# Performance work log

Measured on AMD Instinct MI355X. Metric: run time of the kernel, lower is better.

## Reference

```python
import jax, jax.numpy as jnp
import numpy as np

B, T, H, W, C = 4, 128, 100, 464, 128
VOCAB, EMB, HID = 30000, 300, 600


def lstm(x, Wx, Wh, b):
    # Keras LSTM, gate order i, f, c, o; returns all hidden states [B,T,HID]
    bsz = x.shape[0]
    xg = jnp.einsum('bte,eg->btg', x, Wx) + b  # precompute input contribution

    def step(carry, xg_t):
        h, c = carry
        g = xg_t + h @ Wh
        i, f, cc, o = jnp.split(g, 4, axis=-1)
        c = jax.nn.sigmoid(f) * c + jax.nn.sigmoid(i) * jnp.tanh(cc)
        h = jax.nn.sigmoid(o) * jnp.tanh(c)
        return (h, c), h

    init = (jnp.zeros((bsz, HID), x.dtype), jnp.zeros((bsz, HID), x.dtype))
    _, hs = jax.lax.scan(step, init, jnp.swapaxes(xg, 0, 1))
    return jnp.swapaxes(hs, 0, 1)


def reverse_seq(x, lengths):
    # tf.reverse_sequence: reverse first lengths[b] steps, keep the rest
    t = jnp.arange(x.shape[1])[None, :]
    L = lengths[:, None]
    idx = jnp.where(t < L, L - 1 - t, t)
    return jnp.take_along_axis(x, idx[:, :, None], axis=1)


def conv5(x, w, b):
    y = jax.lax.conv_general_dilated(x, w, (1, 1), 'SAME',
                                     dimension_numbers=('NHWC', 'HWIO', 'NHWC'))
    return jax.nn.relu(y + b)


def deconv5(x, w, b):
    y = jax.lax.conv_transpose(x, w, (1, 1), 'SAME',
                               dimension_numbers=('NHWC', 'HWIO', 'NHWC'))
    return jax.nn.relu(y + b)


def setup_inputs():
    key = jax.random.key(0)
    ks = jax.random.split(key, 30)
    s = 0.05
    p = {}
    p['image_embed'] = jax.random.normal(ks[0], (B, H, W, C), jnp.float32)
    p['instructions'] = jax.random.randint(ks[1], (B, T), 1, VOCAB).astype(jnp.int32)
    p['instruction_lengths'] = jax.random.randint(ks[2], (B,), T // 2, T + 1).astype(jnp.int32)
    p['embed_table'] = jax.random.normal(ks[3], (VOCAB, EMB), jnp.float32) * s
    p['fwd_Wx'] = jax.random.normal(ks[4], (EMB, 4 * HID), jnp.float32) * s
    p['fwd_Wh'] = jax.random.normal(ks[5], (HID, 4 * HID), jnp.float32) * s
    p['fwd_b'] = jnp.zeros((4 * HID,), jnp.float32)
    p['bwd_Wx'] = jax.random.normal(ks[6], (EMB, 4 * HID), jnp.float32) * s
    p['bwd_Wh'] = jax.random.normal(ks[7], (HID, 4 * HID), jnp.float32) * s
    p['bwd_b'] = jnp.zeros((4 * HID,), jnp.float32)
    p['k1_W'] = jax.random.normal(ks[8], (HID, C * C), jnp.float32) * s
    p['k1_b'] = jnp.zeros((C * C,), jnp.float32)
    p['k2_W'] = jax.random.normal(ks[9], (HID, C * C), jnp.float32) * s
    p['k2_b'] = jnp.zeros((C * C,), jnp.float32)
    p['conv1_w'] = jax.random.normal(ks[10], (5, 5, C, C), jnp.float32) * s
    p['conv1_b'] = jnp.zeros((C,), jnp.float32)
    p['conv2_w'] = jax.random.normal(ks[11], (5, 5, C, C), jnp.float32) * s
    p['conv2_b'] = jnp.zeros((C,), jnp.float32)
    p['deconv1_w'] = jax.random.normal(ks[12], (5, 5, 2 * C, C), jnp.float32) * s
    p['deconv1_b'] = jnp.zeros((C,), jnp.float32)
    p['deconv2_w'] = jax.random.normal(ks[13], (5, 5, C, C), jnp.float32) * s
    p['deconv2_b'] = jnp.zeros((C,), jnp.float32)
    p['d1_W'] = jax.random.normal(ks[14], (C, C), jnp.float32) * s
    p['d1_b'] = jnp.zeros((C,), jnp.float32)
    p['d2_W'] = jax.random.normal(ks[15], (C, C), jnp.float32) * s
    p['d2_b'] = jnp.zeros((C,), jnp.float32)
    p['out_W'] = jax.random.normal(ks[16], (C, 1), jnp.float32) * s
    return p


def reference(image_embed, instructions, instruction_lengths, embed_table,
              fwd_Wx, fwd_Wh, fwd_b, bwd_Wx, bwd_Wh, bwd_b,
              k1_W, k1_b, k2_W, k2_b,
              conv1_w, conv1_b, conv2_w, conv2_b,
              deconv1_w, deconv1_b, deconv2_w, deconv2_b,
              d1_W, d1_b, d2_W, d2_b, out_W):
    # --- text encoder ---
    text = embed_table[instructions]  # [B,T,EMB]
    fo = lstm(text, fwd_Wx, fwd_Wh, fwd_b)
    rev = reverse_seq(text, instruction_lengths)
    bo = reverse_seq(lstm(rev, bwd_Wx, bwd_Wh, bwd_b), instruction_lengths)
    outs = jnp.concatenate([fo, bo], axis=-1)  # [B,T,1200]
    mask = (jnp.arange(T)[None, :] < instruction_lengths[:, None]).astype(outs.dtype)
    outs = outs * mask[:, :, None]
    text_embed = jnp.mean(outs, axis=1)  # [B,1200]
    te1, te2 = jnp.split(text_embed, 2, axis=-1)
    # dynamic per-example 1x1 kernels [B,Cin,Cout]
    kern1 = (te1 @ k1_W + k1_b).reshape(B, C, C)
    kern2 = (te2 @ k2_W + k2_b).reshape(B, C, C)
    # --- U-Net ---
    f1 = conv5(image_embed, conv1_w, conv1_b)
    f2 = conv5(f1, conv2_w, conv2_b)
    g1 = jnp.einsum('bhwc,bco->bhwo', f1, kern1)  # parallel 1x1 conv
    g2 = jnp.einsum('bhwc,bco->bhwo', f2, kern2)
    h2 = deconv5(g2, deconv2_w, deconv2_b)
    h1 = deconv5(jnp.concatenate([h2, g1], axis=3), deconv1_w, deconv1_b)
    o1 = jax.nn.relu(h1 @ d1_W + d1_b)
    o2 = jax.nn.relu(o1 @ d2_W + d2_b)
    out = (o2 @ out_W)[..., 0].reshape(B, -1)  # [B, H*W]
    return jax.nn.softmax(out, axis=-1)
```

## Files before the change

### kernel.cpp

```cpp
#include <hip/hip_runtime.h>
#include <cmath>

#define BATCH 4
#define TSEQ  128
#define HH    100
#define WW    464
#define CC    128
#define EMBD  300
#define HIDD  600
#define GATE4 2400
#define NPIX  (HH*WW)
#define IMG   ((size_t)BATCH*NPIX*CC)

#define OFF_A  ((size_t)0)
#define OFF_B  (IMG)
#define OFF_C  (2*IMG)
#define OFF_XG (3*IMG)
#define SZ_XG  ((size_t)2*BATCH*TSEQ*GATE4)
#define OFF_H  (OFF_XG + SZ_XG)
#define SZ_H   ((size_t)2*2*BATCH*HIDD)
#define OFF_CS (OFF_H + SZ_H)
#define SZ_CS  ((size_t)2*BATCH*HIDD)
#define OFF_TS (OFF_CS + SZ_CS)
#define SZ_TS  ((size_t)2*BATCH*HIDD)
#define OFF_K  (OFF_TS + SZ_TS)
#define SZ_K   ((size_t)2*BATCH*CC*CC)
#define OFF_W  (OFF_K + SZ_K)
#define WSLOT  (25*CC*CC)
#define WELEMS (5*WSLOT)

typedef _Float16 f16x8 __attribute__((ext_vector_type(8)));
typedef _Float16 f16x4 __attribute__((ext_vector_type(4)));
typedef float    f32x4 __attribute__((ext_vector_type(4)));

__global__ void zero_f(float* p, int n) {
    int i = blockIdx.x*blockDim.x + threadIdx.x;
    if (i < n) p[i] = 0.f;
}

__global__ void wcvt(const float* __restrict__ c1, const float* __restrict__ c2,
                     const float* __restrict__ dc2, const float* __restrict__ dc1,
                     _Float16* __restrict__ whi, _Float16* __restrict__ wlo)
{
    int e0 = blockIdx.x*256 + threadIdx.x;
    int slot = e0 / WSLOT;
    int r = e0 % WSLOT;
    int tap = r >> 14;
    int idx = r & 16383;
    int e    = idx & 7;
    int lane = (idx >> 3) & 63;
    int ni   = (idx >> 9) & 3;
    int kt   = (idx >> 11) & 3;
    int wn   = (idx >> 13) & 1;
    int l15 = lane & 15, kg = lane >> 4;
    int oc = wn*64 + ni*16 + l15;
    int ic = kt*32 + kg*8 + e;
    const float* s; size_t si;
    if      (slot == 0) { s = c1;  si = ((size_t)tap*128 + ic)*128 + oc; }
    else if (slot == 1) { s = c2;  si = ((size_t)tap*128 + ic)*128 + oc; }
    else if (slot == 2) { s = dc2; si = ((size_t)tap*128 + ic)*128 + oc; }
    else if (slot == 3) { s = dc1; si = ((size_t)tap*256 + ic)*128 + oc; }
    else                { s = dc1; si = ((size_t)tap*256 + 128 + ic)*128 + oc; }
    float v = s[si];
    _Float16 h  = (_Float16)v;
    _Float16 lo = (_Float16)(v - (float)h);
    whi[e0] = h; wlo[e0] = lo;
}

__global__ void wh_t(const float* __restrict__ fWh, const float* __restrict__ bWh,
                     float* __restrict__ whT)
{
    int j = blockIdx.x*256 + threadIdx.x;
    int dir = blockIdx.y;
    if (j >= GATE4) return;
    const float* W = dir ? bWh : fWh;
    float* o = whT + ((size_t)dir*GATE4 + j)*HIDD;
    for (int k = 0; k < HIDD; k += 4) {
        float4 v;
        v.x = W[(size_t)k*GATE4 + j];
        v.y = W[(size_t)(k+1)*GATE4 + j];
        v.z = W[(size_t)(k+2)*GATE4 + j];
        v.w = W[(size_t)(k+3)*GATE4 + j];
        *reinterpret_cast<float4*>(o + k) = v;
    }
}

__global__ void embed_xg(const int* __restrict__ instr, const int* __restrict__ lens,
                         const float* __restrict__ etab,
                         const float* __restrict__ fWx, const float* __restrict__ fb,
                         const float* __restrict__ bWx, const float* __restrict__ bb,
                         float* __restrict__ xg)
{
    int gy  = blockIdx.y;
    int dir = gy >> 5;
    int b   = (gy >> 3) & 3;
    int tt  = gy & 7;
    int t0  = tt*16;
    int j   = blockIdx.x*256 + threadIdx.x;
    __shared__ int tok[16];
    __shared__ __attribute__((aligned(16))) float rows_t[EMBD][16];
    int L = lens[b];
    if (threadIdx.x < 16) {
        int t = t0 + threadIdx.x;
        int tsel = (dir == 1 && t < L) ? (L - 1 - t) : t;
        tok[threadIdx.x] = instr[b*TSEQ + tsel];
    }
    __syncthreads();
    for (int idx = threadIdx.x; idx < 16*EMBD; idx += 256) {
        int k = idx >> 4, r = idx & 15;
        rows_t[k][r] = etab[(size_t)tok[r]*EMBD + k];
    }
    __syncthreads();
    if (j >= GATE4) return;
    const float* Wx   = dir ? bWx : fWx;
    const float* bias = dir ? bb  : fb;
    float bv = bias[j];
    float acc[16];
    #pragma unroll
    for (int r = 0; r < 16; ++r) acc[r] = bv;
    for (int k = 0; k < EMBD; ++k) {
        float w = Wx[(size_t)k*GATE4 + j];
        float4 a0 = *reinterpret_cast<const float4*>(&rows_t[k][0]);
        float4 a1 = *reinterpret_cast<const float4*>(&rows_t[k][4]);
        float4 a2 = *reinterpret_cast<const float4*>(&rows_t[k][8]);
        float4 a3 = *reinterpret_cast<const float4*>(&rows_t[k][12]);
        acc[0]+=a0.x*w;  acc[1]+=a0.y*w;  acc[2]+=a0.z*w;  acc[3]+=a0.w*w;
        acc[4]+=a1.x*w;  acc[5]+=a1.y*w;  acc[6]+=a1.z*w;  acc[7]+=a1.w*w;
        acc[8]+=a2.x*w;  acc[9]+=a2.y*w;  acc[10]+=a2.z*w; acc[11]+=a2.w*w;
        acc[12]+=a3.x*w; acc[13]+=a3.y*w; acc[14]+=a3.z*w; acc[15]+=a3.w*w;
    }
    float* o = xg + ((size_t)(dir*BATCH + b)*TSEQ + t0)*GATE4 + j;
    #pragma unroll
    for (int r = 0; r < 16; ++r) o[(size_t)r*GATE4] = acc[r];
}

__global__ __launch_bounds__(256)
void lstm_step2(const float* __restrict__ xg, const float* __restrict__ whT,
                const int* __restrict__ lens,
                float* __restrict__ hbuf, float* __restrict__ cbuf,
                float* __restrict__ tsum, int t)
{
    int blk = blockIdx.x;
    int dir = blk / 150;
    int u   = (blk % 150)*4 + (threadIdx.x >> 6);
    int lane = threadIdx.x & 63;
    __shared__ float hl[BATCH][HIDD];
    const float* hprev = hbuf + (((size_t)(t&1)*2 + dir)*BATCH)*HIDD;
    for (int i = threadIdx.x; i < BATCH*HIDD; i += 256) hl[i/HIDD][i % HIDD] = hprev[i];
    __syncthreads();
    const float* wr = whT + (size_t)dir*GATE4*HIDD;
    float acc[4][4] = {};
    #pragma unroll
    for (int i = 0; i < 10; ++i) {
        int k = i*64 + lane;
        if (k < HIDD) {
            float h0 = hl[0][k], h1 = hl[1][k], h2 = hl[2][k], h3 = hl[3][k];
            #pragma unroll
            for (int g = 0; g < 4; ++g) {
                float w = wr[(size_t)(g*HIDD + u)*HIDD + k];
                acc[g][0] += w*h0; acc[g][1] += w*h1;
                acc[g][2] += w*h2; acc[g][3] += w*h3;
            }
        }
    }
    #pragma unroll
    for (int off = 32; off; off >>= 1) {
        #pragma unroll
        for (int g = 0; g < 4; ++g) {
            acc[g][0] += __shfl_xor(acc[g][0], off, 64);
            acc[g][1] += __shfl_xor(acc[g][1], off, 64);
            acc[g][2] += __shfl_xor(acc[g][2], off, 64);
            acc[g][3] += __shfl_xor(acc[g][3], off, 64);
        }
    }
    if (lane == 0) {
        #pragma unroll
        for (int b = 0; b < 4; ++b) {
            const float* x = xg + ((size_t)(dir*BATCH + b)*TSEQ + t)*GATE4;
            float ai = x[u]          + acc[0][b];
            float af = x[HIDD + u]   + acc[1][b];
            float ac = x[2*HIDD + u] + acc[2][b];
            float ao = x[3*HIDD + u] + acc[3][b];
            size_t ci = ((size_t)dir*BATCH + b)*HIDD + u;
            float cold = cbuf[ci];
            float si = 1.f/(1.f + expf(-ai));
            float sf = 1.f/(1.f + expf(-af));
            float so = 1.f/(1.f + expf(-ao));
            float cnew = sf*cold + si*tanhf(ac);
            float hnew = so*tanhf(cnew);
            cbuf[ci] = cnew;
            hbuf[(((size_t)((t+1)&1)*2 + dir)*BATCH + b)*HIDD + u] = hnew;
            if (t < lens[b]) tsum[ci] += hnew;
        }
    }
}

__global__ void kern_gemm(const float* __restrict__ tsum,
                          const float* __restrict__ k1W, const float* __restrict__ k1b,
                          const float* __restrict__ k2W, const float* __restrict__ k2b,
                          float* __restrict__ kern)
{
    int which = blockIdx.y;
    int co = blockIdx.x*256 + threadIdx.x;
    __shared__ float te[BATCH][HIDD];
    for (int i = threadIdx.x; i < BATCH*HIDD; i += 256) {
        int b = i / HIDD, k = i % HIDD;
        te[b][k] = tsum[((size_t)which*BATCH + b)*HIDD + k]*(1.f/128.f);
    }
    __syncthreads();
    const float* W    = which ? k2W : k1W;
    const float* bias = which ? k2b : k1b;
    float bv = bias[co];
    float a0=bv, a1=bv, a2=bv, a3=bv;
    for (int k = 0; k < HIDD; ++k) {
        float w = W[(size_t)k*16384 + co];
        a0 += te[0][k]*w; a1 += te[1][k]*w; a2 += te[2][k]*w; a3 += te[3][k]*w;
    }
    kern[((size_t)which*BATCH+0)*16384+co] = a0;
    kern[((size_t)which*BATCH+1)*16384+co] = a1;
    kern[((size_t)which*BATCH+2)*16384+co] = a2;
    kern[((size_t)which*BATCH+3)*16384+co] = a3;
}

template<int MODE>
__global__ __launch_bounds__(256)
void conv5m(const float* __restrict__ src, const _Float16* __restrict__ whi,
            const _Float16* __restrict__ wlo, const float* __restrict__ bias,
            float* __restrict__ dst)
{
    __shared__ _Float16 lds[2*20480];
    const int tid = threadIdx.x;
    const int b  = blockIdx.z;
    const int r0 = blockIdx.y*4, p0 = blockIdx.x*16;
    const size_t rowS = (size_t)WW*CC, imgS = (size_t)HH*rowS;
    const float* sb = src + (size_t)b*imgS;

    for (int it = 0; it < 20; ++it) {
        int idx = it*256 + tid;
        int c4  = idx & 31;
        int px  = (idx >> 5) % 20;
        int row = idx / 640;
        int gr = r0 + row - 2, gp = p0 + px - 2;
        float4 v = make_float4(0.f,0.f,0.f,0.f);
        if ((unsigned)gr < HH && (unsigned)gp < WW)
            v = *reinterpret_cast<const float4*>(sb + (size_t)gr*rowS + (size_t)gp*CC + c4*4);
        int pix = row*20 + px;
        int ph  = (pix*128 + c4*4) ^ ((pix & 7) << 3);
        _Float16 h0=(_Float16)v.x, h1=(_Float16)v.y, h2=(_Float16)v.z, h3=(_Float16)v.w;
        f16x4 hv = {h0, h1, h2, h3};
        f16x4 lv = {(_Float16)(v.x-(float)h0), (_Float16)(v.y-(float)h1),
                    (_Float16)(v.z-(float)h2), (_Float16)(v.w-(float)h3)};
        *reinterpret_cast<f16x4*>(&lds[ph]) = hv;
        *reinterpret_cast<f16x4*>(&lds[20480 + ph]) = lv;
    }
    __syncthreads();

    const int lane = tid & 63, w = tid >> 6;
    const int wm = w & 1, wn = w >> 1;
    const int l15 = lane & 15, kg = lane >> 4;

    f32x4 acc[2][4];
    #pragma unroll
    for (int mi = 0; mi < 2; ++mi)
        #pragma unroll
        for (int ni = 0; ni < 4; ++ni)
            acc[mi][ni] = (f32x4){0.f,0.f,0.f,0.f};

    for (int dy = 0; dy < 5; ++dy) {
        for (int dx = 0; dx < 5; ++dx) {
            const int tap = dy*5 + dx;
            const _Float16* wth = whi + ((size_t)tap << 14) + wn*8192 + lane*8;
            const _Float16* wtl = wlo + ((size_t)tap << 14) + wn*8192 + lane*8;
            int pix0 = (wm*2 + dy)*20 + l15 + dx;
            int a0 = pix0*128 + kg*8;       int sw0 = (pix0 & 7) << 3;
            int pix1 = pix0 + 20;
            int a1 = pix1*128 + kg*8;       int sw1 = (pix1 & 7) << 3;
            for (int kt = 0; kt < 4; ++kt) {
                const _Float16* ph = wth + kt*2048;
                const _Float16* pl = wtl + kt*2048;
                f16x8 bh0 = *(const f16x8*)(ph);
                f16x8 bh1 = *(const f16x8*)(ph + 512);
                f16x8 bh2 = *(const f16x8*)(ph + 1024);
                f16x8 bh3 = *(const f16x8*)(ph + 1536);
                f16x8 bl0 = *(const f16x8*)(pl);
                f16x8 bl1 = *(const f16x8*)(pl + 512);
                f16x8 bl2 = *(const f16x8*)(pl + 1024);
                f16x8 bl3 = *(const f16x8*)(pl + 1536);
                f16x8 ah0 = *(const f16x8*)&lds[(a0 + kt*32) ^ sw0];
                f16x8 al0 = *(const f16x8*)&lds[20480 + ((a0 + kt*32) ^ sw0)];
                f16x8 ah1 = *(const f16x8*)&lds[(a1 + kt*32) ^ sw1];
                f16x8 al1 = *(const f16x8*)&lds[20480 + ((a1 + kt*32) ^ sw1)];
#define SPLIT_MFMA(mi, ni, AH, AL, BH, BL)                                          \
    acc[mi][ni] = __builtin_amdgcn_mfma_f32_16x16x32_f16(AH, BH, acc[mi][ni],0,0,0);\
    acc[mi][ni] = __builtin_amdgcn_mfma_f32_16x16x32_f16(AH, BL, acc[mi][ni],0,0,0);\
    acc[mi][ni] = __builtin_amdgcn_mfma_f32_16x16x32_f16(AL, BH, acc[mi][ni],0,0,0);
                SPLIT_MFMA(0,0, ah0, al0, bh0, bl0)
                SPLIT_MFMA(0,1, ah0, al0, bh1, bl1)
                SPLIT_MFMA(0,2, ah0, al0, bh2, bl2)
                SPLIT_MFMA(0,3, ah0, al0, bh3, bl3)
                SPLIT_MFMA(1,0, ah1, al1, bh0, bl0)
                SPLIT_MFMA(1,1, ah1, al1, bh1, bl1)
                SPLIT_MFMA(1,2, ah1, al1, bh2, bl2)
                SPLIT_MFMA(1,3, ah1, al1, bh3, bl3)
#undef SPLIT_MFMA
            }
        }
    }

    #pragma unroll
    for (int ni = 0; ni < 4; ++ni) {
        int oc = wn*64 + ni*16 + l15;
        float bv = (MODE != 0) ? bias[oc] : 0.f;
        #pragma unroll
        for (int mi = 0; mi < 2; ++mi) {
            float* op = dst + (size_t)b*imgS + (size_t)(r0 + wm*2 + mi)*rowS
                            + (size_t)(p0 + kg*4)*CC + oc;
            f32x4 a = acc[mi][ni];
            #pragma unroll
            for (int q = 0; q < 4; ++q) {
                float v = a[q];
                float* ap = op + (size_t)q*CC;
                if (MODE == 0)      *ap = v;
                else if (MODE == 1) *ap = fmaxf(v + bv, 0.f);
                else                *ap = fmaxf(v + *ap + bv, 0.f);
            }
        }
    }
}

__global__ void chanmul(const float* __restrict__ src, const float* __restrict__ kern,
                        float* __restrict__ dst)
{
    __shared__ float kl[CC*CC];
    int b  = blockIdx.y;
    int p0 = blockIdx.x*32;
    const float* kb = kern + (size_t)b*CC*CC;
    for (int i = threadIdx.x; i < CC*CC/4; i += 256)
        reinterpret_cast<float4*>(kl)[i] = reinterpret_cast<const float4*>(kb)[i];
    __syncthreads();
    int ocg = threadIdx.x & 31, pxg = threadIdx.x >> 5;
    int oc0 = ocg*4;
    const float* xs = src + ((size_t)b*NPIX + p0 + pxg*4)*CC;
    float acc[4][4] = {};
    for (int c = 0; c < CC; ++c) {
        float4 wv = *reinterpret_cast<const float4*>(kl + c*CC + oc0);
        #pragma unroll
        for (int pp = 0; pp < 4; ++pp) {
            float xv = xs[(size_t)pp*CC + c];
            acc[pp][0] += xv*wv.x; acc[pp][1] += xv*wv.y;
            acc[pp][2] += xv*wv.z; acc[pp][3] += xv*wv.w;
        }
    }
    #pragma unroll
    for (int pp = 0; pp < 4; ++pp) {
        float* o = dst + ((size_t)b*NPIX + p0 + pxg*4 + pp)*CC + oc0;
        o[0]=acc[pp][0]; o[1]=acc[pp][1]; o[2]=acc[pp][2]; o[3]=acc[pp][3];
    }
}

__global__ void head(const float* __restrict__ h1,
                     const float* __restrict__ d1W, const float* __restrict__ d1b,
                     const float* __restrict__ d2W, const float* __restrict__ d2b,
                     const float* __restrict__ oW, float* __restrict__ out)
{
    int half = threadIdx.x >> 7;
    int j    = threadIdx.x & 127;
    int px   = blockIdx.x*2 + half;
    __shared__ float xv[2][CC];
    __shared__ float o1[2][CC];
    __shared__ float red[4];
    xv[half][j] = h1[(size_t)px*CC + j];
    __syncthreads();
    float a = d1b[j];
    for (int c = 0; c < CC; ++c) a += xv[half][c]*d1W[c*CC + j];
    a = fmaxf(a, 0.f);
    o1[half][j] = a;
    __syncthreads();
    float a2 = d2b[j];
    for (int c = 0; c < CC; ++c) a2 += o1[half][c]*d2W[c*CC + j];
    a2 = fmaxf(a2, 0.f);
    float contrib = a2*oW[j];
    for (int o = 32; o; o >>= 1) contrib += __shfl_down(contrib, o, 64);
    if ((threadIdx.x & 63) == 0) red[threadIdx.x >> 6] = contrib;
    __syncthreads();
    if (threadIdx.x == 0)   out[px] = red[0] + red[1];
    if (threadIdx.x == 128) out[px] = red[2] + red[3];
}

__global__ void softmax_rows(float* __restrict__ out)
{
    int b = blockIdx.x;
    float* row = out + (size_t)b*NPIX;
    __shared__ float red[16];
    float m = -3.4e38f;
    for (int i = threadIdx.x; i < NPIX; i += 1024) m = fmaxf(m, row[i]);
    for (int o = 32; o; o >>= 1) m = fmaxf(m, __shfl_down(m, o, 64));
    if ((threadIdx.x & 63) == 0) red[threadIdx.x >> 6] = m;
    __syncthreads();
    if (threadIdx.x == 0) {
        float mm = red[0];
        for (int i = 1; i < 16; ++i) mm = fmaxf(mm, red[i]);
        red[0] = mm;
    }
    __syncthreads();
    m = red[0];
    __syncthreads();
    float s = 0.f;
    for (int i = threadIdx.x; i < NPIX; i += 1024) s += expf(row[i] - m);
    for (int o = 32; o; o >>= 1) s += __shfl_down(s, o, 64);
    if ((threadIdx.x & 63) == 0) red[threadIdx.x >> 6] = s;
    __syncthreads();
    if (threadIdx.x == 0) {
        float ss = 0.f;
        for (int i = 0; i < 16; ++i) ss += red[i];
        red[0] = ss;
    }
    __syncthreads();
    float inv = 1.f/red[0];
    for (int i = threadIdx.x; i < NPIX; i += 1024) row[i] = expf(row[i] - m)*inv;
}

extern "C" void kernel_launch(void* const* d_in, const int* in_sizes, int n_in,
                              void* d_out, int out_size, void* d_ws, size_t ws_size,
                              hipStream_t stream) {
    (void)in_sizes; (void)n_in; (void)out_size; (void)ws_size;
    const float* img  = (const float*)d_in[0];
    const int* instr  = (const int*)d_in[1];
    const int* lens   = (const int*)d_in[2];
    const float* etab = (const float*)d_in[3];
    const float* fWx  = (const float*)d_in[4];
    const float* fWh  = (const float*)d_in[5];
    const float* fb   = (const float*)d_in[6];
    const float* bWx  = (const float*)d_in[7];
    const float* bWh  = (const float*)d_in[8];
    const float* bb   = (const float*)d_in[9];
    const float* k1W  = (const float*)d_in[10];
    const float* k1b  = (const float*)d_in[11];
    const float* k2W  = (const float*)d_in[12];
    const float* k2b  = (const float*)d_in[13];
    const float* c1w  = (const float*)d_in[14];
    const float* c1b  = (const float*)d_in[15];
    const float* c2w  = (const float*)d_in[16];
    const float* c2b  = (const float*)d_in[17];
    const float* dc1w = (const float*)d_in[18];
    const float* dc1b = (const float*)d_in[19];
    const float* dc2w = (const float*)d_in[20];
    const float* dc2b = (const float*)d_in[21];
    const float* d1W  = (const float*)d_in[22];
    const float* d1b  = (const float*)d_in[23];
    const float* d2W  = (const float*)d_in[24];
    const float* d2b  = (const float*)d_in[25];
    const float* oW   = (const float*)d_in[26];
    float* out = (float*)d_out;
    float* ws  = (float*)d_ws;

    float* A  = ws + OFF_A;
    float* Bb = ws + OFF_B;
    float* Cb = ws + OFF_C;
    float* xg = ws + OFF_XG;
    float* hb = ws + OFF_H;
    float* cb = ws + OFF_CS;
    float* ts = ws + OFF_TS;
    float* kn = ws + OFF_K;
    _Float16* whi = (_Float16*)(ws + OFF_W);
    _Float16* wlo = whi + WELEMS;
    float* whT = Cb;

    wcvt<<<WELEMS/256, 256, 0, stream>>>(c1w, c2w, dc2w, dc1w, whi, wlo);
    wh_t<<<dim3(10, 2), 256, 0, stream>>>(fWh, bWh, whT);
    zero_f<<<dim3((int)((SZ_H+SZ_CS+SZ_TS+255)/256)), 256, 0, stream>>>(hb, (int)(SZ_H+SZ_CS+SZ_TS));
    embed_xg<<<dim3(10, 64), 256, 0, stream>>>(instr, lens, etab, fWx, fb, bWx, bb, xg);
    for (int t = 0; t < TSEQ; ++t)
        lstm_step2<<<300, 256, 0, stream>>>(xg, whT, lens, hb, cb, ts, t);
    kern_gemm<<<dim3(64, 2), 256, 0, stream>>>(ts, k1W, k1b, k2W, k2b, kn);
    dim3 cgrid(WW/16, HH/4, BATCH);
    conv5m<1><<<cgrid, 256, 0, stream>>>(img, whi + 0*WSLOT, wlo + 0*WSLOT, c1b, A);
    conv5m<1><<<cgrid, 256, 0, stream>>>(A,   whi + 1*WSLOT, wlo + 1*WSLOT, c2b, Bb);
    chanmul<<<dim3(NPIX/32, BATCH), 256, 0, stream>>>(A,  kn, Cb);
    chanmul<<<dim3(NPIX/32, BATCH), 256, 0, stream>>>(Bb, kn + (size_t)BATCH*CC*CC, A);
    conv5m<1><<<cgrid, 256, 0, stream>>>(A,  whi + 2*WSLOT, wlo + 2*WSLOT, dc2b, Bb);
    conv5m<0><<<cgrid, 256, 0, stream>>>(Bb, whi + 3*WSLOT, wlo + 3*WSLOT, dc1b, A);
    conv5m<2><<<cgrid, 256, 0, stream>>>(Cb, whi + 4*WSLOT, wlo + 4*WSLOT, dc1b, A);
    head<<<dim3(BATCH*NPIX/2), 256, 0, stream>>>(A, d1W, d1b, d2W, d2b, oW, out);
    softmax_rows<<<dim3(BATCH), 1024, 0, stream>>>(out);
}
```

Baseline: 5.287 ms.

## Rewrite pointwise MLP head with split-fp16 MFMA matrix instructions

Replaces the scalar per-pixel two-layer MLP head with an MFMA kernel in which each wave processes 32 pixels. It uses hi/lo fp16 splitting with three MFMAs per product to keep near-fp32 accuracy. A new kernel pre-converts the d1/d2 weights into the MFMA fragment layout. The intermediate activations go through swizzled LDS, which uses 64KB per block and may limit occupancy.

```diff
diff --git a/kernel.cpp b/kernel.cpp
--- a/kernel.cpp
+++ b/kernel.cpp
@@ -25,9 +25,10 @@
 #define SZ_TS  ((size_t)2*BATCH*HIDD)
 #define OFF_K  (OFF_TS + SZ_TS)
 #define SZ_K   ((size_t)2*BATCH*CC*CC)
-#define OFF_W  (OFF_K + SZ_K)
+#define OFF_W  (OFF_TS + SZ_TS + SZ_K)
 #define WSLOT  (25*CC*CC)
 #define WELEMS (5*WSLOT)
+#define OFF_WH (OFF_W + WELEMS)
 
 typedef _Float16 f16x8 __attribute__((ext_vector_type(8)));
 typedef _Float16 f16x4 __attribute__((ext_vector_type(4)));
@@ -36,6 +37,16 @@
 __global__ void zero_f(float* p, int n) {
     int i = blockIdx.x*blockDim.x + threadIdx.x;
     if (i < n) p[i] = 0.f;
+}
+
+__device__ __forceinline__ void cvt8(float4 v0, float4 v1, f16x8& h, f16x8& l) {
+    _Float16 h0=(_Float16)v0.x, h1=(_Float16)v0.y, h2=(_Float16)v0.z, h3=(_Float16)v0.w;
+    _Float16 h4=(_Float16)v1.x, h5=(_Float16)v1.y, h6=(_Float16)v1.z, h7=(_Float16)v1.w;
+    h = (f16x8){h0,h1,h2,h3,h4,h5,h6,h7};
+    l = (f16x8){(_Float16)(v0.x-(float)h0), (_Float16)(v0.y-(float)h1),
+                (_Float16)(v0.z-(float)h2), (_Float16)(v0.w-(float)h3),
+                (_Float16)(v1.x-(float)h4), (_Float16)(v1.y-(float)h5),
+                (_Float16)(v1.z-(float)h6), (_Float16)(v1.w-(float)h7)};
 }
 
 __global__ void wcvt(const float* __restrict__ c1, const float* __restrict__ c2,
@@ -65,6 +76,27 @@
     _Float16 h  = (_Float16)v;
     _Float16 lo = (_Float16)(v - (float)h);
     whi[e0] = h; wlo[e0] = lo;
+}
+
+__global__ void wcvt_head(const float* __restrict__ d1W, const float* __restrict__ d2W,
+                          _Float16* __restrict__ whd)
+{
+    int e0 = blockIdx.x*256 + threadIdx.x;
+    int which = e0 >> 14;
+    int idx = e0 & 16383;
+    int e    = idx & 7;
+    int lane = (idx >> 3) & 63;
+    int ni   = (idx >> 9) & 7;
+    int kt   = (idx >> 12) & 3;
+    int l15 = lane & 15, kg = lane >> 4;
+    int oc = ni*16 + l15;
+    int k  = kt*32 + kg*8 + e;
+    const float* W = which ? d2W : d1W;
+    float v = W[(size_t)k*CC + oc];
+    _Float16 h  = (_Float16)v;
+    _Float16 lo = (_Float16)(v - (float)h);
+    whd[(size_t)which*32768 + idx]         = h;
+    whd[(size_t)which*32768 + 16384 + idx] = lo;
 }
 
 __global__ void wh_t(const float* __restrict__ fWh, const float* __restrict__ bWh,
@@ -358,33 +390,119 @@
     }
 }
 
-__global__ void head(const float* __restrict__ h1,
-                     const float* __restrict__ d1W, const float* __restrict__ d1b,
-                     const float* __restrict__ d2W, const float* __restrict__ d2b,
-                     const float* __restrict__ oW, float* __restrict__ out)
-{
-    int half = threadIdx.x >> 7;
-    int j    = threadIdx.x & 127;
-    int px   = blockIdx.x*2 + half;
-    __shared__ float xv[2][CC];
-    __shared__ float o1[2][CC];
-    __shared__ float red[4];
-    xv[half][j] = h1[(size_t)px*CC + j];
-    __syncthreads();
-    float a = d1b[j];
-    for (int c = 0; c < CC; ++c) a += xv[half][c]*d1W[c*CC + j];
-    a = fmaxf(a, 0.f);
-    o1[half][j] = a;
-    __syncthreads();
-    float a2 = d2b[j];
-    for (int c = 0; c < CC; ++c) a2 += o1[half][c]*d2W[c*CC + j];
-    a2 = fmaxf(a2, 0.f);
-    float contrib = a2*oW[j];
-    for (int o = 32; o; o >>= 1) contrib += __shfl_down(contrib, o, 64);
-    if ((threadIdx.x & 63) == 0) red[threadIdx.x >> 6] = contrib;
-    __syncthreads();
-    if (threadIdx.x == 0)   out[px] = red[0] + red[1];
-    if (threadIdx.x == 128) out[px] = red[2] + red[3];
+__global__ __launch_bounds__(256)
+void head_mfma(const float* __restrict__ X, const _Float16* __restrict__ whd,
+               const float* __restrict__ d1b, const float* __restrict__ d2b,
+               const float* __restrict__ oW, float* __restrict__ out)
+{
+    __shared__ float o1s[4][4096];
+    const int tid = threadIdx.x;
+    const int lane = tid & 63, w = tid >> 6;
+    const int l15 = lane & 15, kg = lane >> 4;
+    const size_t pxbase = (size_t)blockIdx.x*128 + w*32;
+    float* o1w = o1s[w];
+
+    const _Float16* w1 = whd;
+    const _Float16* w2 = whd + 32768;
+
+    f32x4 acc[2][8];
+    #pragma unroll
+    for (int ni = 0; ni < 8; ++ni) {
+        float bv = d1b[ni*16 + l15];
+        acc[0][ni] = (f32x4){bv,bv,bv,bv};
+        acc[1][ni] = (f32x4){bv,bv,bv,bv};
+    }
+    #pragma unroll
+    for (int kt = 0; kt < 4; ++kt) {
+        f16x8 ah0, al0, ah1, al1;
+        {
+            const float* xp = X + (pxbase + l15)*CC + kt*32 + kg*8;
+            cvt8(*(const float4*)xp, *(const float4*)(xp+4), ah0, al0);
+            const float* xq = xp + 16*CC;
+            cvt8(*(const float4*)xq, *(const float4*)(xq+4), ah1, al1);
+        }
+        #pragma unroll
+        for (int ni = 0; ni < 8; ++ni) {
+            const _Float16* bp = w1 + (((size_t)kt*8 + ni)*64 + lane)*8;
+            f16x8 bh = *(const f16x8*)bp;
+            f16x8 bl = *(const f16x8*)(bp + 16384);
+            acc[0][ni] = __builtin_amdgcn_mfma_f32_16x16x32_f16(ah0, bh, acc[0][ni],0,0,0);
+            acc[0][ni] = __builtin_amdgcn_mfma_f32_16x16x32_f16(ah0, bl, acc[0][ni],0,0,0);
+            acc[0][ni] = __builtin_amdgcn_mfma_f32_16x16x32_f16(al0, bh, acc[0][ni],0,0,0);
+            acc[1][ni] = __builtin_amdgcn_mfma_f32_16x16x32_f16(ah1, bh, acc[1][ni],0,0,0);
+            acc[1][ni] = __builtin_amdgcn_mfma_f32_16x16x32_f16(ah1, bl, acc[1][ni],0,0,0);
+            acc[1][ni] = __builtin_amdgcn_mfma_f32_16x16x32_f16(al1, bh, acc[1][ni],0,0,0);
+        }
+    }
+    #pragma unroll
+    for (int mi = 0; mi < 2; ++mi)
+        #pragma unroll
+        for (int ni = 0; ni < 8; ++ni) {
+            f32x4 a = acc[mi][ni];
+            #pragma unroll
+            for (int q = 0; q < 4; ++q) {
+                int px = mi*16 + kg*4 + q;
+                int oc = ni*16 + l15;
+                o1w[(px*128 + oc) ^ ((px & 7) << 3)] = fmaxf(a[q], 0.f);
+            }
+        }
+
+    f32x4 acc2[2][8];
+    #pragma unroll
+    for (int ni = 0; ni < 8; ++ni) {
+        float bv = d2b[ni*16 + l15];
+        acc2[0][ni] = (f32x4){bv,bv,bv,bv};
+        acc2[1][ni] = (f32x4){bv,bv,bv,bv};
+    }
+    #pragma unroll
+    for (int kt = 0; kt < 4; ++kt) {
+        f16x8 ah0, al0, ah1, al1;
+        {
+            int px0 = l15;
+            int i0 = (px0*128 + kt*32 + kg*8) ^ ((px0 & 7) << 3);
+            cvt8(*(const float4*)&o1w[i0], *(const float4*)&o1w[i0+4], ah0, al0);
+            int px1 = 16 + l15;
+            int i1 = (px1*128 + kt*32 + kg*8) ^ ((px1 & 7) << 3);
+            cvt8(*(const float4*)&o1w[i1], *(const float4*)&o1w[i1+4], ah1, al1);
+        }
+        #pragma unroll
+        for (int ni = 0; ni < 8; ++ni) {
+            const _Float16* bp = w2 + (((size_t)kt*8 + ni)*64 + lane)*8;
+            f16x8 bh = *(const f16x8*)bp;
+            f16x8 bl = *(const f16x8*)(bp + 16384);
+            acc2[0][ni] = __builtin_amdgcn_mfma_f32_16x16x32_f16(ah0, bh, acc2[0][ni],0,0,0);
+            acc2[0][ni] = __builtin_amdgcn_mfma_f32_16x16x32_f16(ah0, bl, acc2[0][ni],0,0,0);
+            acc2[0][ni] = __builtin_amdgcn_mfma_f32_16x16x32_f16(al0, bh, acc2[0][ni],0,0,0);
+            acc2[1][ni] = __builtin_amdgcn_mfma_f32_16x16x32_f16(ah1, bh, acc2[1][ni],0,0,0);
+            acc2[1][ni] = __builtin_amdgcn_mfma_f32_16x16x32_f16(ah1, bl, acc2[1][ni],0,0,0);
+            acc2[1][ni] = __builtin_amdgcn_mfma_f32_16x16x32_f16(al1, bh, acc2[1][ni],0,0,0);
+        }
+    }
+
+    #pragma unroll
+    for (int mi = 0; mi < 2; ++mi) {
+        float p0 = 0.f, p1 = 0.f, p2 = 0.f, p3 = 0.f;
+        #pragma unroll
+        for (int ni = 0; ni < 8; ++ni) {
+            float ow = oW[ni*16 + l15];
+            f32x4 a = acc2[mi][ni];
+            p0 += fmaxf(a[0], 0.f)*ow;
+            p1 += fmaxf(a[1], 0.f)*ow;
+            p2 += fmaxf(a[2], 0.f)*ow;
+            p3 += fmaxf(a[3], 0.f)*ow;
+        }
+        #pragma unroll
+        for (int off = 1; off < 16; off <<= 1) {
+            p0 += __shfl_xor(p0, off, 64);
+            p1 += __shfl_xor(p1, off, 64);
+            p2 += __shfl_xor(p2, off, 64);
+            p3 += __shfl_xor(p3, off, 64);
+        }
+        if (l15 == 0) {
+            float* op = out + pxbase + mi*16 + kg*4;
+            op[0] = p0; op[1] = p1; op[2] = p2; op[3] = p3;
+        }
+    }
 }
 
 __global__ void softmax_rows(float* __restrict__ out)
@@ -464,9 +582,11 @@
     float* kn = ws + OFF_K;
     _Float16* whi = (_Float16*)(ws + OFF_W);
     _Float16* wlo = whi + WELEMS;
+    _Float16* whd = (_Float16*)(ws + OFF_WH);
     float* whT = Cb;
 
     wcvt<<<WELEMS/256, 256, 0, stream>>>(c1w, c2w, dc2w, dc1w, whi, wlo);
+    wcvt_head<<<128, 256, 0, stream>>>(d1W, d2W, whd);
     wh_t<<<dim3(10, 2), 256, 0, stream>>>(fWh, bWh, whT);
     zero_f<<<dim3((int)((SZ_H+SZ_CS+SZ_TS+255)/256)), 256, 0, stream>>>(hb, (int)(SZ_H+SZ_CS+SZ_TS));
     embed_xg<<<dim3(10, 64), 256, 0, stream>>>(instr, lens, etab, fWx, fb, bWx, bb, xg);
@@ -481,6 +601,6 @@
     conv5m<1><<<cgrid, 256, 0, stream>>>(A,  whi + 2*WSLOT, wlo + 2*WSLOT, dc2b, Bb);
     conv5m<0><<<cgrid, 256, 0, stream>>>(Bb, whi + 3*WSLOT, wlo + 3*WSLOT, dc1b, A);
     conv5m<2><<<cgrid, 256, 0, stream>>>(Cb, whi + 4*WSLOT, wlo + 4*WSLOT, dc1b, A);
-    head<<<dim3(BATCH*NPIX/2), 256, 0, stream>>>(A, d1W, d1b, d2W, d2b, oW, out);
+    head_mfma<<<1450, 256, 0, stream>>>(A, whd, d1b, d2b, oW, out);
     softmax_rows<<<dim3(BATCH), 1024, 0, stream>>>(out);
 }
```

Measured after the change: 4.704 ms. 1.12x faster.
